# Kernel tuning notes

Hardware: AMD Instinct MI355X
Metric: run time of the kernel (lower is better)

## Reference

```python
import jax, jax.numpy as jnp
import numpy as np


def setup_inputs() -> dict:
    key = jax.random.key(0)
    k1, k2, k3 = jax.random.split(key, 3)
    B, C, D, H, W = 4, 64, 32, 64, 64
    x = jax.random.normal(k1, (B, C, D, H, W), dtype=jnp.float32)
    # Conv3d(in=2, out=1, k=7), PyTorch default init: U(-s, s), s = 1/sqrt(fan_in)
    fan_in = 2 * 7 * 7 * 7
    s = 1.0 / np.sqrt(fan_in)
    conv_w = jax.random.uniform(k2, (1, 2, 7, 7, 7), dtype=jnp.float32, minval=-s, maxval=s)
    conv_b = jax.random.uniform(k3, (1,), dtype=jnp.float32, minval=-s, maxval=s)
    return {"x": x, "conv_w": conv_w, "conv_b": conv_b}


def reference(x, conv_w, conv_b):
    # channel-wise max and mean -> [B, 2, D, H, W]
    xc = jnp.stack([jnp.max(x, axis=1), jnp.mean(x, axis=1)], axis=1)
    # conv3d 2->1, k7, stride 1, padding 3 (SAME)
    y = jax.lax.conv_general_dilated(
        xc, conv_w,
        window_strides=(1, 1, 1),
        padding=[(3, 3), (3, 3), (3, 3)],
        dimension_numbers=("NCDHW", "OIDHW", "NCDHW"),
    ) + conv_b[None, :, None, None, None]
    scale = jax.nn.sigmoid(y)  # [B, 1, D, H, W]
    return x * scale
```

## Files before the change

kernel.cpp:

```cpp
#include <hip/hip_runtime.h>
#include <math.h>

#define B_ 4
#define C_ 64
#define D_ 32
#define H_ 64
#define W_ 64
#define S_ (D_*H_*W_)
#define S4_ (S_/4)
#define HW_ (H_*W_)

typedef float floatx4 __attribute__((ext_vector_type(4)));

__global__ __launch_bounds__(256) void reduce_kernel(const float* __restrict__ x,
                                                     float* __restrict__ xc) {
    int i  = blockIdx.x * 256 + threadIdx.x;
    int b  = i >> 15;
    int s4 = i & (S4_ - 1);
    const float4* x4 = reinterpret_cast<const float4*>(x) + (size_t)b * C_ * S4_ + s4;
    float4 v = x4[0];
    float mx0 = v.x, mx1 = v.y, mx2 = v.z, mx3 = v.w;
    float sm0 = v.x, sm1 = v.y, sm2 = v.z, sm3 = v.w;
    #pragma unroll 8
    for (int c = 1; c < C_; ++c) {
        float4 t = x4[(size_t)c * S4_];
        mx0 = fmaxf(mx0, t.x); sm0 += t.x;
        mx1 = fmaxf(mx1, t.y); sm1 += t.y;
        mx2 = fmaxf(mx2, t.z); sm2 += t.z;
        mx3 = fmaxf(mx3, t.w); sm3 += t.w;
    }
    float4* o = reinterpret_cast<float4*>(xc);
    float4 a; a.x = mx0; a.y = mx1; a.z = mx2; a.w = mx3;
    o[((size_t)b * 2 + 0) * S4_ + s4] = a;
    const float inv = 1.0f / 64.0f;
    float4 m; m.x = sm0 * inv; m.y = sm1 * inv; m.z = sm2 * inv; m.w = sm3 * inv;
    o[((size_t)b * 2 + 1) * S4_ + s4] = m;
}

#define ZT 8
#define YT 14
#define XS 72
#define PLANE (YT*XS)
#define CHSZ (ZT*PLANE)
#define HALO_N (2*ZT*YT*70)

__global__ __launch_bounds__(256, 2) void conv_gate_kernel(const float* __restrict__ xc,
                                                           const float* __restrict__ x,
                                                           const float* __restrict__ cw,
                                                           const float* __restrict__ cb,
                                                           float* __restrict__ out) {
    __shared__ __align__(16) float tile[2 * CHSZ];

    const int tid = threadIdx.x;
    const int b  = blockIdx.z >> 4;
    const int d0 = (blockIdx.z & 15) * 2;
    const int h0 = blockIdx.y * 8;

    const int w4 = tid & 15;
    const int hh = (tid >> 4) & 7;
    const int dd = tid >> 7;

    for (int base = tid; base < HALO_N; base += 256 * 8) {
        float sv[8];
        int   sa[8];
        #pragma unroll
        for (int k = 0; k < 8; ++k) {
            int idx = base + k * 256;
            sv[k] = 0.f;
            sa[k] = -1;
            if (idx < HALO_N) {
                int ch = idx / 7840;
                int r  = idx - ch * 7840;
                int z  = r / 980;
                int r2 = r - z * 980;
                int y  = r2 / 70;
                int xw = r2 - y * 70;
                sa[k] = ch * CHSZ + z * PLANE + y * XS + xw;
                int gd = d0 + z - 3, gh = h0 + y - 3, gw = xw - 3;
                if ((unsigned)gd < (unsigned)D_ && (unsigned)gh < (unsigned)H_ &&
                    (unsigned)gw < (unsigned)W_)
                    sv[k] = xc[(size_t)(b * 2 + ch) * S_ + gd * HW_ + gh * W_ + gw];
            }
        }
        #pragma unroll
        for (int k = 0; k < 8; ++k)
            if (sa[k] >= 0) tile[sa[k]] = sv[k];
    }

    const int h = h0 + hh, w = w4 * 4;
    const size_t sp = (size_t)(d0 + dd) * HW_ + (size_t)h * W_ + w;
    const float* xp = x + (size_t)b * C_ * S_ + sp;
    float* op = out + (size_t)b * C_ * S_ + sp;
    floatx4 v0[16];
    #pragma unroll
    for (int k = 0; k < 16; ++k)
        v0[k] = *reinterpret_cast<const floatx4*>(xp + (size_t)k * S_);

    __syncthreads();

    float acc[4] = {0.f, 0.f, 0.f, 0.f};
    for (int ch = 0; ch < 2; ++ch) {
        const float* tch = &tile[ch * CHSZ + dd * PLANE + w4 * 4];
        const float* wch = cw + ch * 343;
        for (int ky = 0; ky < 7; ++ky) {
            const float* trow = tch + (hh + ky) * XS;
            const float* wky  = wch + ky * 7;
            #pragma unroll
            for (int kz = 0; kz < 7; ++kz) {
                const float* rp = trow + kz * PLANE;
                float4 f0 = *reinterpret_cast<const float4*>(rp);
                float4 f1 = *reinterpret_cast<const float4*>(rp + 4);
                float2 f2 = *reinterpret_cast<const float2*>(rp + 8);
                float win[10] = {f0.x, f0.y, f0.z, f0.w,
                                 f1.x, f1.y, f1.z, f1.w, f2.x, f2.y};
                const float* wr = wky + kz * 49;
                float wc[7];
                #pragma unroll
                for (int k = 0; k < 7; ++k) wc[k] = wr[k];
                #pragma unroll
                for (int kw = 0; kw < 7; ++kw) {
                    acc[0] = fmaf(win[kw + 0], wc[kw], acc[0]);
                    acc[1] = fmaf(win[kw + 1], wc[kw], acc[1]);
                    acc[2] = fmaf(win[kw + 2], wc[kw], acc[2]);
                    acc[3] = fmaf(win[kw + 3], wc[kw], acc[3]);
                }
            }
        }
    }

    const float bias = cb[0];
    floatx4 s0;
    s0.x = 1.0f / (1.0f + __expf(-(acc[0] + bias)));
    s0.y = 1.0f / (1.0f + __expf(-(acc[1] + bias)));
    s0.z = 1.0f / (1.0f + __expf(-(acc[2] + bias)));
    s0.w = 1.0f / (1.0f + __expf(-(acc[3] + bias)));

    #pragma unroll
    for (int k = 0; k < 16; ++k)
        *reinterpret_cast<floatx4*>(op + (size_t)k * S_) = v0[k] * s0;
    for (int c = 16; c < C_; c += 16) {
        floatx4 v[16];
        #pragma unroll
        for (int k = 0; k < 16; ++k)
            v[k] = *reinterpret_cast<const floatx4*>(xp + (size_t)(c + k) * S_);
        #pragma unroll
        for (int k = 0; k < 16; ++k)
            *reinterpret_cast<floatx4*>(op + (size_t)(c + k) * S_) = v[k] * s0;
    }
}

extern "C" void kernel_launch(void* const* d_in, const int* in_sizes, int n_in,
                              void* d_out, int out_size, void* d_ws, size_t ws_size,
                              hipStream_t stream) {
    const float* x  = (const float*)d_in[0];
    const float* cw = (const float*)d_in[1];
    const float* cb = (const float*)d_in[2];
    float* out = (float*)d_out;
    float* xc  = (float*)d_ws;

    reduce_kernel<<<dim3((B_ * S4_) / 256), dim3(256), 0, stream>>>(x, xc);
    conv_gate_kernel<<<dim3(1, H_ / 8, B_ * (D_ / 2)), dim3(256), 0, stream>>>(
        xc, x, cw, cb, out);
}
```

Before: 85.20 us.

## Compute two output rows per thread in conv with register row reuse, share scales via LDS

The conv stage now runs on half the threads (two waves), each computing two adjacent output rows so every loaded LDS row feeds two accumulators, roughly halving LDS reads per output. The sigmoid scales are written to shared memory and broadcast back to all 256 threads for the gating pass. The prefetch/stream chunk for x is cut from 16 to 8 channels to reduce register pressure. The cost is idle waves during the conv phase, an extra barrier, and less memory-level parallelism in the streaming loop.

```diff
diff --git a/kernel.cpp b/kernel.cpp
--- a/kernel.cpp
+++ b/kernel.cpp
@@ -56,9 +56,9 @@
     const int d0 = (blockIdx.z & 15) * 2;
     const int h0 = blockIdx.y * 8;
 
-    const int w4 = tid & 15;
-    const int hh = (tid >> 4) & 7;
-    const int dd = tid >> 7;
+    const int sw4 = tid & 15;
+    const int shh = (tid >> 4) & 7;
+    const int sdd = tid >> 7;
 
     for (int base = tid; base < HALO_N; base += 256 * 8) {
         float sv[8];
@@ -87,65 +87,96 @@
             if (sa[k] >= 0) tile[sa[k]] = sv[k];
     }
 
-    const int h = h0 + hh, w = w4 * 4;
-    const size_t sp = (size_t)(d0 + dd) * HW_ + (size_t)h * W_ + w;
+    const size_t sp = (size_t)(d0 + sdd) * HW_ + (size_t)(h0 + shh) * W_ + sw4 * 4;
     const float* xp = x + (size_t)b * C_ * S_ + sp;
     float* op = out + (size_t)b * C_ * S_ + sp;
-    floatx4 v0[16];
+    floatx4 v0[8];
     #pragma unroll
-    for (int k = 0; k < 16; ++k)
+    for (int k = 0; k < 8; ++k)
         v0[k] = *reinterpret_cast<const floatx4*>(xp + (size_t)k * S_);
 
     __syncthreads();
 
-    float acc[4] = {0.f, 0.f, 0.f, 0.f};
-    for (int ch = 0; ch < 2; ++ch) {
-        const float* tch = &tile[ch * CHSZ + dd * PLANE + w4 * 4];
-        const float* wch = cw + ch * 343;
-        for (int ky = 0; ky < 7; ++ky) {
-            const float* trow = tch + (hh + ky) * XS;
-            const float* wky  = wch + ky * 7;
-            #pragma unroll
+    floatx4 s0, s1;
+    const int cw4 = tid & 15;
+    const int chg = (tid >> 4) & 3;
+    const int cdd = (tid >> 6) & 1;
+    if (tid < 128) {
+        float acc0[4] = {0.f, 0.f, 0.f, 0.f};
+        float acc1[4] = {0.f, 0.f, 0.f, 0.f};
+        for (int ch = 0; ch < 2; ++ch) {
+            const float* tch = &tile[ch * CHSZ + cdd * PLANE + cw4 * 4];
+            const float* wch = cw + ch * 343;
             for (int kz = 0; kz < 7; ++kz) {
-                const float* rp = trow + kz * PLANE;
-                float4 f0 = *reinterpret_cast<const float4*>(rp);
-                float4 f1 = *reinterpret_cast<const float4*>(rp + 4);
-                float2 f2 = *reinterpret_cast<const float2*>(rp + 8);
-                float win[10] = {f0.x, f0.y, f0.z, f0.w,
-                                 f1.x, f1.y, f1.z, f1.w, f2.x, f2.y};
-                const float* wr = wky + kz * 49;
-                float wc[7];
+                const float* trow = tch + kz * PLANE + (chg * 2) * XS;
+                const float* wkz  = wch + kz * 49;
+                float wp[7];
                 #pragma unroll
-                for (int k = 0; k < 7; ++k) wc[k] = wr[k];
-                #pragma unroll
-                for (int kw = 0; kw < 7; ++kw) {
-                    acc[0] = fmaf(win[kw + 0], wc[kw], acc[0]);
-                    acc[1] = fmaf(win[kw + 1], wc[kw], acc[1]);
-                    acc[2] = fmaf(win[kw + 2], wc[kw], acc[2]);
-                    acc[3] = fmaf(win[kw + 3], wc[kw], acc[3]);
+                for (int r = 0; r < 8; ++r) {
+                    const float* rp = trow + r * XS;
+                    float4 f0 = *reinterpret_cast<const float4*>(rp);
+                    float4 f1 = *reinterpret_cast<const float4*>(rp + 4);
+                    float2 f2 = *reinterpret_cast<const float2*>(rp + 8);
+                    float win[10] = {f0.x, f0.y, f0.z, f0.w,
+                                     f1.x, f1.y, f1.z, f1.w, f2.x, f2.y};
+                    if (r >= 1) {
+                        #pragma unroll
+                        for (int kw = 0; kw < 7; ++kw) {
+                            acc1[0] = fmaf(win[kw + 0], wp[kw], acc1[0]);
+                            acc1[1] = fmaf(win[kw + 1], wp[kw], acc1[1]);
+                            acc1[2] = fmaf(win[kw + 2], wp[kw], acc1[2]);
+                            acc1[3] = fmaf(win[kw + 3], wp[kw], acc1[3]);
+                        }
+                    }
+                    if (r < 7) {
+                        const float* wr = wkz + r * 7;
+                        float wc[7];
+                        #pragma unroll
+                        for (int k = 0; k < 7; ++k) wc[k] = wr[k];
+                        #pragma unroll
+                        for (int kw = 0; kw < 7; ++kw) {
+                            acc0[0] = fmaf(win[kw + 0], wc[kw], acc0[0]);
+                            acc0[1] = fmaf(win[kw + 1], wc[kw], acc0[1]);
+                            acc0[2] = fmaf(win[kw + 2], wc[kw], acc0[2]);
+                            acc0[3] = fmaf(win[kw + 3], wc[kw], acc0[3]);
+                        }
+                        #pragma unroll
+                        for (int k = 0; k < 7; ++k) wp[k] = wc[k];
+                    }
                 }
             }
         }
+        const float bias = cb[0];
+        s0.x = 1.0f / (1.0f + __expf(-(acc0[0] + bias)));
+        s0.y = 1.0f / (1.0f + __expf(-(acc0[1] + bias)));
+        s0.z = 1.0f / (1.0f + __expf(-(acc0[2] + bias)));
+        s0.w = 1.0f / (1.0f + __expf(-(acc0[3] + bias)));
+        s1.x = 1.0f / (1.0f + __expf(-(acc1[0] + bias)));
+        s1.y = 1.0f / (1.0f + __expf(-(acc1[1] + bias)));
+        s1.z = 1.0f / (1.0f + __expf(-(acc1[2] + bias)));
+        s1.w = 1.0f / (1.0f + __expf(-(acc1[3] + bias)));
     }
+    __syncthreads();
 
-    const float bias = cb[0];
-    floatx4 s0;
-    s0.x = 1.0f / (1.0f + __expf(-(acc[0] + bias)));
-    s0.y = 1.0f / (1.0f + __expf(-(acc[1] + bias)));
-    s0.z = 1.0f / (1.0f + __expf(-(acc[2] + bias)));
-    s0.w = 1.0f / (1.0f + __expf(-(acc[3] + bias)));
+    floatx4* scl = reinterpret_cast<floatx4*>(tile);
+    if (tid < 128) {
+        scl[(cdd * 8 + chg * 2 + 0) * 16 + cw4] = s0;
+        scl[(cdd * 8 + chg * 2 + 1) * 16 + cw4] = s1;
+    }
+    __syncthreads();
 
+    const floatx4 sc = scl[(sdd * 8 + shh) * 16 + sw4];
     #pragma unroll
-    for (int k = 0; k < 16; ++k)
-        *reinterpret_cast<floatx4*>(op + (size_t)k * S_) = v0[k] * s0;
-    for (int c = 16; c < C_; c += 16) {
-        floatx4 v[16];
+    for (int k = 0; k < 8; ++k)
+        *reinterpret_cast<floatx4*>(op + (size_t)k * S_) = v0[k] * sc;
+    for (int c = 8; c < C_; c += 8) {
+        floatx4 v[8];
         #pragma unroll
-        for (int k = 0; k < 16; ++k)
+        for (int k = 0; k < 8; ++k)
             v[k] = *reinterpret_cast<const floatx4*>(xp + (size_t)(c + k) * S_);
         #pragma unroll
-        for (int k = 0; k < 16; ++k)
-            *reinterpret_cast<floatx4*>(op + (size_t)(c + k) * S_) = v[k] * s0;
+        for (int k = 0; k < 8; ++k)
+            *reinterpret_cast<floatx4*>(op + (size_t)(c + k) * S_) = v[k] * sc;
     }
 }
 
```

New measurement: 83.51 us. -2.0%, faster.
